# Kernel tuning notes

Measured on AMD Instinct MI355X. Metric: run time of the kernel, lower is better.

## Reference

```python
import jax, jax.numpy as jnp
import numpy as np

EPS = 1e-9
LDIM = 4  # dim_g + dim_t + dim_b + dim_w


def _mvn_logpdf(v, F):
    # batched zero-mean multivariate normal log-density, v: (N,O), F: (N,O,O)
    chol = jnp.linalg.cholesky(F)
    z = jax.scipy.linalg.solve_triangular(chol, v[..., None], lower=True)[..., 0]
    quad = jnp.sum(z * z, axis=-1)
    logdet = 2.0 * jnp.sum(jnp.log(jnp.diagonal(chol, axis1=-2, axis2=-1)), axis=-1)
    k = v.shape[-1]
    return -0.5 * (quad + logdet + k * jnp.log(2.0 * jnp.pi))


def _forward(y, B_G, B_T, B_B, B_W, lambda_r1_free, lambda_r2_free,
             q_diag, r_diag, gamma1, gamma2_learnable):
    N, Nt, O = y.shape
    L = LDIM
    # ----- _build_matrices -----
    B11 = jnp.zeros((L, L)).at[0, 0].set(B_G[0, 0]).at[1, 1].set(B_T[0, 0]).at[2, 2].set(B_B[0, 0])
    B22 = jnp.zeros((L, L)).at[3, 3].set(B_W[0, 0])
    B12 = jnp.zeros((L, L)).at[3, :3].set(1.0 / 3.0)  # regime1 factors feed shared factor
    B21 = jnp.zeros((L, L))
    L1 = jnp.zeros((O, L))
    L1 = L1.at[0, 0].set(1.0).at[1, 0].set(lambda_r1_free[0]).at[2, 0].set(lambda_r1_free[1])
    L1 = L1.at[3, 1].set(1.0).at[4, 1].set(lambda_r1_free[2]).at[5, 1].set(lambda_r1_free[3])
    L1 = L1.at[6, 2].set(1.0).at[7, 2].set(lambda_r1_free[4]).at[8, 2].set(lambda_r1_free[5])
    L2 = jnp.zeros((O, L)).at[0, 3].set(1.0).at[1:, 3].set(lambda_r2_free)
    Q = jnp.diag(jnp.abs(q_diag) + 1e-4)
    R = jnp.diag(jnp.abs(r_diag) + 1e-4)
    F_JIT = 1e-5 * jnp.eye(O)
    I_L = jnp.eye(L)
    P22_CONST = 0.9999

    # ----- initial beliefs ('informative') -----
    prob0 = jnp.tile(jnp.array([0.99, 0.01], jnp.float32), (N, 1))
    eta0 = jnp.zeros((N, L), y.dtype)
    P0 = jnp.tile(jnp.diag(jnp.array([1000.0, 1000.0, 1000.0, 1e-9], y.dtype))[None], (N, 1, 1))

    def predict(B, eta, P):
        # eta: (N,L), P: (N,L,L)
        return eta @ B.T, jnp.einsum('ij,njk,lk->nil', B, P, B) + Q

    def innov(Lm, e, Pp, y_t):
        v = y_t - e @ Lm.T
        F = jnp.einsum('oi,nij,pj->nop', Lm, Pp, Lm) + R + F_JIT
        return v, F

    def kupdate(e, Pp, Lm, v, F):
        LP = jnp.einsum('oi,nij->noj', Lm, Pp)          # (N,O,L)
        K = jnp.swapaxes(jnp.linalg.solve(F, LP), -1, -2)  # P Lm^T F^{-1}, (N,L,O)
        e_u = e + jnp.einsum('nlo,no->nl', K, v)
        IKL = I_L - K @ Lm                                # (N,L,L)
        P_u = IKL @ Pp @ jnp.swapaxes(IKL, -1, -2) + jnp.einsum('nlo,op,nmp->nlm', K, R, K)
        return e_u, P_u

    def collapse(w_a, w_b, e_a, e_b, P_a, P_b):
        e = w_a[:, None] * e_a + w_b[:, None] * e_b
        da, db = e_a - e, e_b - e
        P = (w_a[:, None, None] * (P_a + da[:, :, None] * da[:, None, :])
             + w_b[:, None, None] * (P_b + db[:, :, None] * db[:, None, :]))
        return e, P

    def step(carry, y_t):
        prob, eta1, eta2, P1, P2, ll = carry
        # HMM transition: p11 depends on regime-1 state (first L-1 components)
        logit_p11 = gamma1 + eta1[:, :3] @ gamma2_learnable
        p11 = jax.nn.sigmoid(logit_p11)
        # predictions for the 4 regime transitions (origin -> destination)
        e11, Pp11 = predict(B11, eta1, P1)
        e12, Pp12 = predict(B21, eta2, P2)
        e21, Pp21 = predict(B12, eta1, P1)
        e22, Pp22 = predict(B22, eta2, P2)
        v11, F11 = innov(L1, e11, Pp11, y_t)
        v12, F12 = innov(L1, e12, Pp12, y_t)
        v21, F21 = innov(L2, e21, Pp21, y_t)
        v22, F22 = innov(L2, e22, Pp22, y_t)
        ll11 = _mvn_logpdf(v11, F11)
        ll12 = _mvn_logpdf(v12, F12)
        ll21 = _mvn_logpdf(v21, F21)
        ll22 = _mvn_logpdf(v22, F22)
        lp = jnp.log(prob + EPS)
        c11 = lp[:, 0] + jnp.log(p11 + EPS) + ll11
        c12 = lp[:, 1] + np.log(1.0 - P22_CONST + EPS) + ll12
        c21 = lp[:, 0] + jnp.log(1.0 - p11 + EPS) + ll21
        c22 = lp[:, 1] + np.log(P22_CONST + EPS) + ll22
        logp = jnp.stack([c11, c12, c21, c22], axis=1)
        ll_t = jax.scipy.special.logsumexp(logp, axis=1)
        pt = jnp.exp(logp - ll_t[:, None])
        pr1 = pt[:, 0] + pt[:, 1]
        pr2 = pt[:, 2] + pt[:, 3]
        W11 = pt[:, 0] / (pr1 + EPS)
        W12 = pt[:, 1] / (pr1 + EPS)
        W21 = pt[:, 2] / (pr2 + EPS)
        W22 = pt[:, 3] / (pr2 + EPS)
        eu11, Pu11 = kupdate(e11, Pp11, L1, v11, F11)
        eu12, Pu12 = kupdate(e12, Pp12, L1, v12, F12)
        eu21, Pu21 = kupdate(e21, Pp21, L2, v21, F21)
        eu22, Pu22 = kupdate(e22, Pp22, L2, v22, F22)
        eta1n, P1n = collapse(W11, W12, eu11, eu12, Pu11, Pu12)
        eta2n, P2n = collapse(W21, W22, eu21, eu22, Pu21, Pu22)
        probn = jnp.stack([pr1, pr2], axis=1)
        return (probn, eta1n, eta2n, P1n, P2n, ll + ll_t.sum()), None

    carry0 = (prob0, eta0, eta0, P0, P0, jnp.zeros((), y.dtype))
    (_, _, _, _, _, total_ll), _ = jax.lax.scan(step, carry0, jnp.swapaxes(y, 0, 1))
    return total_ll


def setup_inputs() -> dict:
    key = jax.random.key(0)
    ks = jax.random.split(key, 12)
    N, Nt, O = 16384, 64, 9
    f32 = jnp.float32
    return {
        'y': jax.random.normal(ks[0], (N, Nt, O), f32),
        'B_G': jax.random.uniform(ks[1], (1, 1), f32, 0.6, 0.95),  # Beta(5,1.5)-like AR coeffs
        'B_T': jax.random.uniform(ks[2], (1, 1), f32, 0.6, 0.95),
        'B_B': jax.random.uniform(ks[3], (1, 1), f32, 0.6, 0.95),
        'B_W': jax.random.uniform(ks[4], (1, 1), f32, 0.6, 0.95),
        'lambda_r1_free': jax.random.normal(ks[5], (6,), f32),
        'lambda_r2_free': jax.random.normal(ks[6], (O - 1,), f32),
        'q_diag': jax.random.uniform(ks[7], (LDIM,), f32),
        'r_diag': jax.random.uniform(ks[8], (O,), f32),
        'gamma1': jnp.abs(jax.random.normal(ks[9], (), f32)),
        'gamma2_learnable': jax.random.normal(ks[10], (LDIM - 1,), f32),
    }


def reference(y, B_G, B_T, B_B, B_W, lambda_r1_free, lambda_r2_free,
              q_diag, r_diag, gamma1, gamma2_learnable):
    return _forward(y, B_G, B_T, B_B, B_W, lambda_r1_free, lambda_r2_free,
                    q_diag, r_diag, gamma1, gamma2_learnable)
```

## Files before the change

### kernel.cpp

```cpp
#include <hip/hip_runtime.h>


static __device__ __forceinline__ float frcp(float x)  { return __builtin_amdgcn_rcpf(x); }
static __device__ __forceinline__ float frsq(float x)  { return __builtin_amdgcn_rsqf(x); }
static __device__ __forceinline__ float fexp2(float x) { return __builtin_amdgcn_exp2f(x); }
static __device__ __forceinline__ float flog2(float x) { return __builtin_amdgcn_logf(x); }

#define EPSF   1e-9f
#define L2E    1.4426950408889634f
#define LN2    0.6931471805599453f
#define L2_2PI_9 23.86346461225016f
#define C12F   1.00001e-4f
#define P22F   0.99990001f
#define QK     (-0.5f * L2E)

__global__ __launch_bounds__(64, 1)
void kf_kernel(const float* __restrict__ y,
               const float* __restrict__ pBG, const float* __restrict__ pBT,
               const float* __restrict__ pBB, const float* __restrict__ pBW,
               const float* __restrict__ lam1, const float* __restrict__ lam2,
               const float* __restrict__ qd,  const float* __restrict__ rd,
               const float* __restrict__ pG1, const float* __restrict__ pG2,
               float* __restrict__ partial, int N, int Nt)
{
    const int lane = threadIdx.x;
    const int sid  = blockIdx.x * 64 + lane;
    const bool valid = (sid < N);
    const int rowlen = Nt * 9;

    const float bg = pBG[0], bt = pBT[0], bb = pBB[0], bw = pBW[0];
    const float a1 = lam1[0], a2 = lam1[1];
    const float a4 = lam1[2], a5 = lam1[3];
    const float a7 = lam1[4], a8 = lam1[5];
    float l2v[9], id[9], ld[9];
    l2v[0] = 1.f;
    #pragma unroll
    for (int i = 0; i < 8; ++i) l2v[i + 1] = lam2[i];
    float l2detD = 0.f;
    #pragma unroll
    for (int o = 0; o < 9; ++o) {
        float dv = fabsf(rd[o]) + 1.0e-4f + 1.0e-5f;
        id[o] = 1.0f / dv;
        ld[o] = l2v[o] * id[o];
        l2detD += flog2(dv);
    }
    const float id0 = id[0], id1 = id[1], id2 = id[2],
                id3 = id[3], id4 = id[4], id5 = id[5],
                id6 = id[6], id7 = id[7], id8 = id[8];
    const float ld0 = ld[0], ld1 = ld[1], ld2 = ld[2],
                ld3 = ld[3], ld4 = ld[4], ld5 = ld[5],
                ld6 = ld[6], ld7 = ld[7], ld8 = ld[8];
    const float aid0 = id0,      aid1 = a1 * id1, aid2 = a2 * id2;
    const float aid3 = id3,      aid4 = a4 * id4, aid5 = a5 * id5;
    const float aid6 = id6,      aid7 = a7 * id7, aid8 = a8 * id8;
    const float q0 = fabsf(qd[0]) + 1e-4f, q1 = fabsf(qd[1]) + 1e-4f;
    const float q2 = fabsf(qd[2]) + 1e-4f, q3 = fabsf(qd[3]) + 1e-4f;
    const float g0 = id0 + a1*a1*id1 + a2*a2*id2;
    const float g1 = id3 + a4*a4*id4 + a5*a5*id5;
    const float g2 = id6 + a7*a7*id7 + a8*a8*id8;
    float h = 0.f;
    #pragma unroll
    for (int o = 0; o < 9; ++o) h += l2v[o] * ld[o];
    const float pk0 = q0 / (1.f + q0 * g0);
    const float pk1 = q1 / (1.f + q1 * g1);
    const float pk2 = q2 / (1.f + q2 * g2);
    const float C12D = C12F * frsq((1.f + q0*g0) * (1.f + q1*g1) * (1.f + q2*g2));
    const float gam1 = pG1[0], w0c = pG2[0], w1c = pG2[1], w2c = pG2[2];
    const float CC = -0.5f * (l2detD + L2_2PI_9);
    const float bg2 = bg*bg, bt2 = bt*bt, bb2 = bb*bb, bw2 = bw*bw;
    const float bgbt = bg*bt, bgbb = bg*bb, btbb = bt*bb;

    float pf1 = 0.99f + EPSF, pf2 = 0.01f + EPSF;
    float se0 = 0.f, se1 = 0.f, se2 = 0.f;
    float p00 = 1000.f, p01 = 0.f, p02 = 0.f, p11 = 1000.f, p12 = 0.f, p22 = 1000.f;
    float sm2 = 0.f, sp2 = 1e-9f;
    float acc2 = 0.f;

    const float* row = y + (size_t)(valid ? sid : 0) * rowlen;
    float A[9], B[9];
    #pragma unroll
    for (int k = 0; k < 9; ++k) A[k] = row[k];

    auto step = [&](const float (&Y)[9]) {
        float logit = gam1 + w0c*se0 + w1c*se1 + w2c*se2;
        float p11s = frcp(1.f + fexp2(-logit * L2E));
        float pf11 = p11s + EPSF, pf21 = 1.f - p11s + EPSF;

        float e0 = bg*se0, e1 = bt*se1, e2 = bb*se2;
        float s00 = bg2*p00 + q0, s11 = bt2*p11 + q1, s22 = bb2*p22 + q2;
        float s01 = bgbt*p01, s02 = bgbb*p02, s12 = btbb*p12;

        float v0 = Y[0] - e0,    v1 = Y[1] - a1*e0, v2 = Y[2] - a2*e0;
        float v3 = Y[3] - e1,    v4 = Y[4] - a4*e1, v5 = Y[5] - a5*e1;
        float v6 = Y[6] - e2,    v7 = Y[7] - a7*e2, v8 = Y[8] - a8*e2;
        float u0 = aid0*v0 + aid1*v1 + aid2*v2;
        float u1 = aid3*v3 + aid4*v4 + aid5*v5;
        float u2 = aid6*v6 + aid7*v7 + aid8*v8;
        float vdv = (id0*v0)*v0 + (id1*v1)*v1 + (id2*v2)*v2
                  + (id3*v3)*v3 + (id4*v4)*v4 + (id5*v5)*v5
                  + (id6*v6)*v6 + (id7*v7)*v7 + (id8*v8)*v8;
        float yl  = ld0*Y[0] + ld1*Y[1] + ld2*Y[2]
                  + ld3*Y[3] + ld4*Y[4] + ld5*Y[5]
                  + ld6*Y[6] + ld7*Y[7] + ld8*Y[8];
        float k0 = 2.f*u0 + g0*e0, k1 = 2.f*u1 + g1*e1, k2 = 2.f*u2 + g2*e2;
        float ydy = vdv + e0*k0 + e1*k1 + e2*k2;

        float m00 = s00*g0 + 1.f, m01 = s01*g1,       m02 = s02*g2;
        float m10 = s01*g0,       m11 = s11*g1 + 1.f, m12 = s12*g2;
        float m20 = s02*g0,       m21 = s12*g1,       m22 = s22*g2 + 1.f;
        float c00 = m11*m22 - m12*m21;
        float c01 = m12*m20 - m10*m22;
        float c02 = m10*m21 - m11*m20;
        float c10 = m02*m21 - m01*m22;
        float c11 = m00*m22 - m02*m20;
        float c12 = m01*m20 - m00*m21;
        float c20 = m01*m12 - m02*m11;
        float c21 = m02*m10 - m00*m12;
        float c22 = m00*m11 - m01*m10;
        float det = m00*c00 + m01*c01 + m02*c02;
        float rs  = frsq(det);
        float iM  = rs * rs;
        float Ci00 = (s00*c00 + s01*c10 + s02*c20) * iM;
        float Ci01 = (s00*c01 + s01*c11 + s02*c21) * iM;
        float Ci02 = (s00*c02 + s01*c12 + s02*c22) * iM;
        float Ci11 = (s01*c01 + s11*c11 + s12*c21) * iM;
        float Ci12 = (s01*c02 + s11*c12 + s12*c22) * iM;
        float Ci22 = (s02*c02 + s12*c12 + s22*c22) * iM;

        float t0 = Ci00*u0 + Ci01*u1 + Ci02*u2;
        float t1 = Ci01*u0 + Ci11*u1 + Ci12*u2;
        float t2 = Ci02*u0 + Ci12*u1 + Ci22*u2;
        float quad11 = vdv - (u0*t0 + u1*t1 + u2*t2);
        float eu0 = e0 + t0, eu1 = e1 + t1, eu2 = e2 + t2;

        float u120 = u0 + g0*e0, u121 = u1 + g1*e1, u122 = u2 + g2*e2;
        float f0 = pk0*u120, f1 = pk1*u121, f2 = pk2*u122;
        float quad12 = ydy - (f0*u120 + f1*u121 + f2*u122);

        float seS = se0 + se1 + se2;
        float sPs = p00 + p11 + p22 + 2.f*(p01 + p02 + p12);
        float m2a = seS * (1.f/3.f);
        float m2b = bw * sm2;
        float pva = q3 + sPs * (1.f/9.f);
        float pvb = bw2*sp2 + q3;
        float u1a = yl - m2a*h;
        float u1b = yl - m2b*h;
        float vdaa = ydy - m2a*(2.f*yl - m2a*h);
        float vdab = ydy - m2b*(2.f*yl - m2b*h);
        float rva = frsq(1.f + pva*h);
        float rvb = frsq(1.f + pvb*h);
        float pua = pva*(rva*rva);
        float pub = pvb*(rvb*rvb);
        float quad21 = vdaa - pua*u1a*u1a;
        float quad22 = vdab - pub*u1b*u1b;
        float eua = m2a + pua*u1a;
        float eub = m2b + pub*u1b;

        float q11e = QK*quad11, q12e = QK*quad12;
        float q21e = QK*quad21, q22e = QK*quad22;
        float Mq = fmaxf(fmaxf(q11e, q12e), fmaxf(q21e, q22e));
        float w11 = pf1*pf11*rs   * fexp2(q11e - Mq);
        float w12 = pf2*C12D      * fexp2(q12e - Mq);
        float w21 = pf1*pf21*rva  * fexp2(q21e - Mq);
        float w22 = pf2*P22F*rvb  * fexp2(q22e - Mq);
        float ssum = (w11 + w12) + (w21 + w22);
        acc2 += Mq + flog2(ssum);
        float pr1n = w11 + w12, pr2n = w21 + w22;
        float inv1 = frcp(pr1n + EPSF*ssum);
        float inv2 = frcp(pr2n + EPSF*ssum);
        float issum = frcp(ssum);
        float W11 = w11*inv1, W12 = w12*inv1;
        float W21 = w21*inv2, W22 = w22*inv2;
        pf1 = pr1n*issum + EPSF;
        pf2 = pr2n*issum + EPSF;

        float ne0 = W11*eu0 + W12*f0;
        float ne1 = W11*eu1 + W12*f1;
        float ne2 = W11*eu2 + W12*f2;
        float da0 = eu0-ne0, da1 = eu1-ne1, da2 = eu2-ne2;
        float db0 = f0-ne0,  db1 = f1-ne1,  db2 = f2-ne2;
        p00 = W11*(Ci00 + da0*da0) + W12*(pk0 + db0*db0);
        p01 = W11*(Ci01 + da0*da1) + W12*(db0*db1);
        p02 = W11*(Ci02 + da0*da2) + W12*(db0*db2);
        p11 = W11*(Ci11 + da1*da1) + W12*(pk1 + db1*db1);
        p12 = W11*(Ci12 + da1*da2) + W12*(db1*db2);
        p22 = W11*(Ci22 + da2*da2) + W12*(pk2 + db2*db2);
        se0 = ne0; se1 = ne1; se2 = ne2;

        float nm2 = W21*eua + W22*eub;
        float dc = eua-nm2, dd = eub-nm2;
        sp2 = W21*(pua + dc*dc) + W22*(pub + dd*dd);
        sm2 = nm2;
    };

    for (int t = 0; t < Nt; t += 2) {
        #pragma unroll
        for (int k = 0; k < 9; ++k) B[k] = row[(t+1)*9 + k];
        step(A);
        if (t + 2 < Nt) {
            #pragma unroll
            for (int k = 0; k < 9; ++k) A[k] = row[(t+2)*9 + k];
        }
        step(B);
    }

    float acc = valid ? (acc2 + (float)Nt * CC) * LN2 : 0.f;
    #pragma unroll
    for (int off = 32; off; off >>= 1) acc += __shfl_down(acc, off, 64);
    if (lane == 0) partial[blockIdx.x] = acc;
}

__global__ __launch_bounds__(64)
void reduce_k(const float* __restrict__ part, float* __restrict__ out, int nb)
{
    float s = 0.f;
    for (int i = threadIdx.x; i < nb; i += 64) s += part[i];
    #pragma unroll
    for (int off = 32; off; off >>= 1) s += __shfl_down(s, off, 64);
    if (threadIdx.x == 0) out[0] = s;
}

extern "C" void kernel_launch(void* const* d_in, const int* in_sizes, int n_in,
                              void* d_out, int out_size, void* d_ws, size_t ws_size,
                              hipStream_t stream)
{
    const float* y    = (const float*)d_in[0];
    const float* pBG  = (const float*)d_in[1];
    const float* pBT  = (const float*)d_in[2];
    const float* pBB  = (const float*)d_in[3];
    const float* pBW  = (const float*)d_in[4];
    const float* lam1 = (const float*)d_in[5];
    const float* lam2 = (const float*)d_in[6];
    const float* qd   = (const float*)d_in[7];
    const float* rd   = (const float*)d_in[8];
    const float* pG1  = (const float*)d_in[9];
    const float* pG2  = (const float*)d_in[10];

    const int total = in_sizes[0];
    const int Nt = 64, O = 9;
    const int N = total / (Nt * O);
    const int blocks = (N + 63) / 64;

    float* partial = (float*)d_ws;
    kf_kernel<<<blocks, 64, 0, stream>>>(y, pBG, pBT, pBB, pBW, lam1, lam2,
                                         qd, rd, pG1, pG2, partial, N, Nt);
    reduce_k<<<1, 64, 0, stream>>>(partial, (float*)d_out, blocks);
}
```

Before: 130.4 us.

## Precompute state-independent observation terms off the recurrence and use packed float2 math

```diff
diff --git a/kernel.cpp b/kernel.cpp
--- a/kernel.cpp
+++ b/kernel.cpp
@@ -1,10 +1,15 @@
 #include <hip/hip_runtime.h>
 
+
+typedef float v2f __attribute__((ext_vector_type(2)));
+typedef v2f v2fu __attribute__((aligned(4)));
 
 static __device__ __forceinline__ float frcp(float x)  { return __builtin_amdgcn_rcpf(x); }
 static __device__ __forceinline__ float frsq(float x)  { return __builtin_amdgcn_rsqf(x); }
 static __device__ __forceinline__ float fexp2(float x) { return __builtin_amdgcn_exp2f(x); }
 static __device__ __forceinline__ float flog2(float x) { return __builtin_amdgcn_logf(x); }
+static __device__ __forceinline__ v2f sp(float x) { return (v2f){x, x}; }
+static __device__ __forceinline__ v2f rsq2(v2f a) { return (v2f){frsq(a.x), frsq(a.y)}; }
 
 #define EPSF   1e-9f
 #define L2E    1.4426950408889634f
@@ -44,20 +49,19 @@
         ld[o] = l2v[o] * id[o];
         l2detD += flog2(dv);
     }
-    const float id0 = id[0], id1 = id[1], id2 = id[2],
-                id3 = id[3], id4 = id[4], id5 = id[5],
-                id6 = id[6], id7 = id[7], id8 = id[8];
-    const float ld0 = ld[0], ld1 = ld[1], ld2 = ld[2],
-                ld3 = ld[3], ld4 = ld[4], ld5 = ld[5],
-                ld6 = ld[6], ld7 = ld[7], ld8 = ld[8];
-    const float aid0 = id0,      aid1 = a1 * id1, aid2 = a2 * id2;
-    const float aid3 = id3,      aid4 = a4 * id4, aid5 = a5 * id5;
-    const float aid6 = id6,      aid7 = a7 * id7, aid8 = a8 * id8;
+    const float id8 = id[8], ld8 = ld[8];
+    const v2f idv01 = {id[0], id[1]}, idv23 = {id[2], id[3]},
+              idv45 = {id[4], id[5]}, idv67 = {id[6], id[7]};
+    const v2f ldv01 = {ld[0], ld[1]}, ldv23 = {ld[2], ld[3]},
+              ldv45 = {ld[4], ld[5]}, ldv67 = {ld[6], ld[7]};
+    const float aid0 = id[0],    aid1 = a1*id[1], aid2 = a2*id[2];
+    const float aid3 = id[3],    aid4 = a4*id[4], aid5 = a5*id[5];
+    const float aid6 = id[6],    aid7 = a7*id[7], aid8 = a8*id[8];
     const float q0 = fabsf(qd[0]) + 1e-4f, q1 = fabsf(qd[1]) + 1e-4f;
     const float q2 = fabsf(qd[2]) + 1e-4f, q3 = fabsf(qd[3]) + 1e-4f;
-    const float g0 = id0 + a1*a1*id1 + a2*a2*id2;
-    const float g1 = id3 + a4*a4*id4 + a5*a5*id5;
-    const float g2 = id6 + a7*a7*id7 + a8*a8*id8;
+    const float g0 = id[0] + a1*a1*id[1] + a2*a2*id[2];
+    const float g1 = id[3] + a4*a4*id[4] + a5*a5*id[5];
+    const float g2 = id[6] + a7*a7*id[7] + a8*a8*id[8];
     float h = 0.f;
     #pragma unroll
     for (int o = 0; o < 9; ++o) h += l2v[o] * ld[o];
@@ -69,6 +73,7 @@
     const float CC = -0.5f * (l2detD + L2_2PI_9);
     const float bg2 = bg*bg, bt2 = bt*bt, bb2 = bb*bb, bw2 = bw*bw;
     const float bgbt = bg*bt, bgbb = bg*bb, btbb = bt*bb;
+    const v2f hv = {h, h};
 
     float pf1 = 0.99f + EPSF, pf2 = 0.01f + EPSF;
     float se0 = 0.f, se1 = 0.f, se2 = 0.f;
@@ -76,132 +81,142 @@
     float sm2 = 0.f, sp2 = 1e-9f;
     float acc2 = 0.f;
 
-    const float* row = y + (size_t)(valid ? sid : 0) * rowlen;
-    float A[9], B[9];
-    #pragma unroll
-    for (int k = 0; k < 9; ++k) A[k] = row[k];
-
-    auto step = [&](const float (&Y)[9]) {
-        float logit = gam1 + w0c*se0 + w1c*se1 + w2c*se2;
-        float p11s = frcp(1.f + fexp2(-logit * L2E));
-        float pf11 = p11s + EPSF, pf21 = 1.f - p11s + EPSF;
+    struct Yr { v2f ab, cd, ef, gh; float i8; };
+    struct YB { float uy0, uy1, uy2, yl, ydy, f0, f1, f2, q12e; };
+
+    const char* rowb = (const char*)(y + (size_t)(valid ? sid : 0) * rowlen);
+    auto loadY = [&](Yr& r, int t) {
+        const char* p = rowb + t * 36;
+        r.ab = *(const v2fu*)(p);
+        r.cd = *(const v2fu*)(p + 8);
+        r.ef = *(const v2fu*)(p + 16);
+        r.gh = *(const v2fu*)(p + 24);
+        r.i8 = *(const float*)(p + 32);
+    };
+    auto computeYB = [&](const Yr& r) {
+        YB o;
+        v2f m0 = idv01*r.ab, m1 = idv23*r.cd, m2 = idv45*r.ef, m3 = idv67*r.gh;
+        v2f yq = m0*r.ab + m1*r.cd + m2*r.ef + m3*r.gh;
+        o.ydy = fmaf(id8*r.i8, r.i8, yq.x + yq.y);
+        v2f la = ldv01*r.ab + ldv23*r.cd + ldv45*r.ef + ldv67*r.gh;
+        o.yl = fmaf(ld8, r.i8, la.x + la.y);
+        o.uy0 = fmaf(aid2, r.cd.x, fmaf(aid1, r.ab.y, aid0*r.ab.x));
+        o.uy1 = fmaf(aid5, r.ef.y, fmaf(aid4, r.ef.x, aid3*r.cd.y));
+        o.uy2 = fmaf(aid8, r.i8,   fmaf(aid7, r.gh.y, aid6*r.gh.x));
+        o.f0 = pk0*o.uy0; o.f1 = pk1*o.uy1; o.f2 = pk2*o.uy2;
+        o.q12e = QK * (o.ydy - (o.f0*o.uy0 + o.f1*o.uy1 + o.f2*o.uy2));
+        return o;
+    };
+
+    auto step = [&](const YB& yb) {
+        float logit = fmaf(w2c, se2, fmaf(w1c, se1, fmaf(w0c, se0, gam1)));
+        float p11s = frcp(1.f + fexp2(-L2E * logit));
+        float pp1 = pf1 * (p11s + EPSF);
+        float pp2 = pf1 * (1.f - p11s + EPSF);
 
         float e0 = bg*se0, e1 = bt*se1, e2 = bb*se2;
-        float s00 = bg2*p00 + q0, s11 = bt2*p11 + q1, s22 = bb2*p22 + q2;
+        float s00 = fmaf(bg2, p00, q0), s11 = fmaf(bt2, p11, q1), s22 = fmaf(bb2, p22, q2);
         float s01 = bgbt*p01, s02 = bgbb*p02, s12 = btbb*p12;
 
-        float v0 = Y[0] - e0,    v1 = Y[1] - a1*e0, v2 = Y[2] - a2*e0;
-        float v3 = Y[3] - e1,    v4 = Y[4] - a4*e1, v5 = Y[5] - a5*e1;
-        float v6 = Y[6] - e2,    v7 = Y[7] - a7*e2, v8 = Y[8] - a8*e2;
-        float u0 = aid0*v0 + aid1*v1 + aid2*v2;
-        float u1 = aid3*v3 + aid4*v4 + aid5*v5;
-        float u2 = aid6*v6 + aid7*v7 + aid8*v8;
-        float vdv = (id0*v0)*v0 + (id1*v1)*v1 + (id2*v2)*v2
-                  + (id3*v3)*v3 + (id4*v4)*v4 + (id5*v5)*v5
-                  + (id6*v6)*v6 + (id7*v7)*v7 + (id8*v8)*v8;
-        float yl  = ld0*Y[0] + ld1*Y[1] + ld2*Y[2]
-                  + ld3*Y[3] + ld4*Y[4] + ld5*Y[5]
-                  + ld6*Y[6] + ld7*Y[7] + ld8*Y[8];
-        float k0 = 2.f*u0 + g0*e0, k1 = 2.f*u1 + g1*e1, k2 = 2.f*u2 + g2*e2;
-        float ydy = vdv + e0*k0 + e1*k1 + e2*k2;
-
-        float m00 = s00*g0 + 1.f, m01 = s01*g1,       m02 = s02*g2;
-        float m10 = s01*g0,       m11 = s11*g1 + 1.f, m12 = s12*g2;
-        float m20 = s02*g0,       m21 = s12*g1,       m22 = s22*g2 + 1.f;
-        float c00 = m11*m22 - m12*m21;
-        float c01 = m12*m20 - m10*m22;
-        float c02 = m10*m21 - m11*m20;
-        float c10 = m02*m21 - m01*m22;
-        float c11 = m00*m22 - m02*m20;
-        float c12 = m01*m20 - m00*m21;
-        float c20 = m01*m12 - m02*m11;
-        float c21 = m02*m10 - m00*m12;
-        float c22 = m00*m11 - m01*m10;
-        float det = m00*c00 + m01*c01 + m02*c02;
+        float u0 = fmaf(-g0, e0, yb.uy0);
+        float u1 = fmaf(-g1, e1, yb.uy1);
+        float u2 = fmaf(-g2, e2, yb.uy2);
+        float vdv = yb.ydy - (e0*(yb.uy0+u0) + e1*(yb.uy1+u1) + e2*(yb.uy2+u2));
+
+        float m00 = fmaf(s00, g0, 1.f), m11 = fmaf(s11, g1, 1.f), m22 = fmaf(s22, g2, 1.f);
+        float m01 = s01*g1, m02 = s02*g2;
+        float m10 = s01*g0, m20 = s02*g0;
+        float m12 = s12*g2, m21 = s12*g1;
+        float c00 = fmaf(m11, m22, -m12*m21);
+        float c01 = fmaf(m12, m20, -m10*m22);
+        float c02 = fmaf(m10, m21, -m11*m20);
+        float c10 = fmaf(m02, m21, -m01*m22);
+        float c11 = fmaf(m00, m22, -m02*m20);
+        float c12 = fmaf(m01, m20, -m00*m21);
+        float c20 = fmaf(m01, m12, -m02*m11);
+        float c21 = fmaf(m02, m10, -m00*m12);
+        float c22 = fmaf(m00, m11, -m01*m10);
+        float det = fmaf(m02, c02, fmaf(m01, c01, m00*c00));
         float rs  = frsq(det);
         float iM  = rs * rs;
-        float Ci00 = (s00*c00 + s01*c10 + s02*c20) * iM;
-        float Ci01 = (s00*c01 + s01*c11 + s02*c21) * iM;
-        float Ci02 = (s00*c02 + s01*c12 + s02*c22) * iM;
-        float Ci11 = (s01*c01 + s11*c11 + s12*c21) * iM;
-        float Ci12 = (s01*c02 + s11*c12 + s12*c22) * iM;
-        float Ci22 = (s02*c02 + s12*c12 + s22*c22) * iM;
-
-        float t0 = Ci00*u0 + Ci01*u1 + Ci02*u2;
-        float t1 = Ci01*u0 + Ci11*u1 + Ci12*u2;
-        float t2 = Ci02*u0 + Ci12*u1 + Ci22*u2;
-        float quad11 = vdv - (u0*t0 + u1*t1 + u2*t2);
-        float eu0 = e0 + t0, eu1 = e1 + t1, eu2 = e2 + t2;
-
-        float u120 = u0 + g0*e0, u121 = u1 + g1*e1, u122 = u2 + g2*e2;
-        float f0 = pk0*u120, f1 = pk1*u121, f2 = pk2*u122;
-        float quad12 = ydy - (f0*u120 + f1*u121 + f2*u122);
+        float SC00 = fmaf(s02, c20, fmaf(s01, c10, s00*c00));
+        float SC01 = fmaf(s02, c21, fmaf(s01, c11, s00*c01));
+        float SC02 = fmaf(s02, c22, fmaf(s01, c12, s00*c02));
+        float SC11 = fmaf(s12, c21, fmaf(s11, c11, s01*c01));
+        float SC12 = fmaf(s12, c22, fmaf(s11, c12, s01*c02));
+        float SC22 = fmaf(s22, c22, fmaf(s12, c12, s02*c02));
+
+        float n0 = fmaf(SC02, u2, fmaf(SC01, u1, SC00*u0));
+        float n1 = fmaf(SC12, u2, fmaf(SC11, u1, SC01*u0));
+        float n2 = fmaf(SC22, u2, fmaf(SC12, u1, SC02*u0));
+        float un = fmaf(u2, n2, fmaf(u1, n1, u0*n0));
+        float quad11 = fmaf(-iM, un, vdv);
+        float eu0 = fmaf(iM, n0, e0), eu1 = fmaf(iM, n1, e1), eu2 = fmaf(iM, n2, e2);
 
         float seS = se0 + se1 + se2;
-        float sPs = p00 + p11 + p22 + 2.f*(p01 + p02 + p12);
-        float m2a = seS * (1.f/3.f);
-        float m2b = bw * sm2;
-        float pva = q3 + sPs * (1.f/9.f);
-        float pvb = bw2*sp2 + q3;
-        float u1a = yl - m2a*h;
-        float u1b = yl - m2b*h;
-        float vdaa = ydy - m2a*(2.f*yl - m2a*h);
-        float vdab = ydy - m2b*(2.f*yl - m2b*h);
-        float rva = frsq(1.f + pva*h);
-        float rvb = frsq(1.f + pvb*h);
-        float pua = pva*(rva*rva);
-        float pub = pvb*(rvb*rvb);
-        float quad21 = vdaa - pua*u1a*u1a;
-        float quad22 = vdab - pub*u1b*u1b;
-        float eua = m2a + pua*u1a;
-        float eub = m2b + pub*u1b;
-
-        float q11e = QK*quad11, q12e = QK*quad12;
-        float q21e = QK*quad21, q22e = QK*quad22;
-        float Mq = fmaxf(fmaxf(q11e, q12e), fmaxf(q21e, q22e));
-        float w11 = pf1*pf11*rs   * fexp2(q11e - Mq);
-        float w12 = pf2*C12D      * fexp2(q12e - Mq);
-        float w21 = pf1*pf21*rva  * fexp2(q21e - Mq);
-        float w22 = pf2*P22F*rvb  * fexp2(q22e - Mq);
-        float ssum = (w11 + w12) + (w21 + w22);
+        float sPs = fmaf(2.f, (p01 + p02) + p12, (p00 + p11) + p22);
+        v2f m2v; m2v.x = seS * (1.f/3.f);          m2v.y = bw * sm2;
+        v2f pvv; pvv.x = fmaf(sPs, 1.f/9.f, q3);   pvv.y = fmaf(bw2, sp2, q3);
+        v2f ylv = sp(yb.yl);
+        v2f u1v = ylv - m2v*hv;
+        v2f vdav = sp(yb.ydy) - m2v*(sp(2.f*yb.yl) - m2v*hv);
+        v2f denv = sp(1.f) + pvv*hv;
+        v2f rv  = rsq2(denv);
+        v2f puv = pvv*(rv*rv);
+        v2f pu1 = puv*u1v;
+        v2f quadv = vdav - pu1*u1v;
+        v2f euv = m2v + pu1;
+
+        float q11e = QK*quad11;
+        float q21e = QK*quadv.x, q22e = QK*quadv.y;
+        float Mq = fmaxf(fmaxf(q11e, yb.q12e), fmaxf(q21e, q22e));
+        float w11 = pp1*rs        * fexp2(q11e - Mq);
+        float w12 = pf2*C12D      * fexp2(yb.q12e - Mq);
+        float w21 = pp2*rv.x      * fexp2(q21e - Mq);
+        float w22 = pf2*P22F*rv.y * fexp2(q22e - Mq);
+        float pr1n = w11 + w12, pr2n = w21 + w22;
+        float ssum = pr1n + pr2n;
         acc2 += Mq + flog2(ssum);
-        float pr1n = w11 + w12, pr2n = w21 + w22;
-        float inv1 = frcp(pr1n + EPSF*ssum);
-        float inv2 = frcp(pr2n + EPSF*ssum);
+        float inv1 = frcp(fmaf(EPSF, ssum, pr1n));
+        float inv2 = frcp(fmaf(EPSF, ssum, pr2n));
         float issum = frcp(ssum);
         float W11 = w11*inv1, W12 = w12*inv1;
         float W21 = w21*inv2, W22 = w22*inv2;
-        pf1 = pr1n*issum + EPSF;
-        pf2 = pr2n*issum + EPSF;
-
-        float ne0 = W11*eu0 + W12*f0;
-        float ne1 = W11*eu1 + W12*f1;
-        float ne2 = W11*eu2 + W12*f2;
+        pf1 = fmaf(pr1n, issum, EPSF);
+        pf2 = fmaf(pr2n, issum, EPSF);
+        float W11i = W11 * iM;
+
+        float ne0 = fmaf(W12, yb.f0, W11*eu0);
+        float ne1 = fmaf(W12, yb.f1, W11*eu1);
+        float ne2 = fmaf(W12, yb.f2, W11*eu2);
         float da0 = eu0-ne0, da1 = eu1-ne1, da2 = eu2-ne2;
-        float db0 = f0-ne0,  db1 = f1-ne1,  db2 = f2-ne2;
-        p00 = W11*(Ci00 + da0*da0) + W12*(pk0 + db0*db0);
-        p01 = W11*(Ci01 + da0*da1) + W12*(db0*db1);
-        p02 = W11*(Ci02 + da0*da2) + W12*(db0*db2);
-        p11 = W11*(Ci11 + da1*da1) + W12*(pk1 + db1*db1);
-        p12 = W11*(Ci12 + da1*da2) + W12*(db1*db2);
-        p22 = W11*(Ci22 + da2*da2) + W12*(pk2 + db2*db2);
+        float db0 = yb.f0-ne0, db1 = yb.f1-ne1, db2 = yb.f2-ne2;
+        p00 = fmaf(W12, fmaf(db0, db0, pk0), fmaf(W11, da0*da0, W11i*SC00));
+        p01 = fmaf(W12, db0*db1,             fmaf(W11, da0*da1, W11i*SC01));
+        p02 = fmaf(W12, db0*db2,             fmaf(W11, da0*da2, W11i*SC02));
+        p11 = fmaf(W12, fmaf(db1, db1, pk1), fmaf(W11, da1*da1, W11i*SC11));
+        p12 = fmaf(W12, db1*db2,             fmaf(W11, da1*da2, W11i*SC12));
+        p22 = fmaf(W12, fmaf(db2, db2, pk2), fmaf(W11, da2*da2, W11i*SC22));
         se0 = ne0; se1 = ne1; se2 = ne2;
 
-        float nm2 = W21*eua + W22*eub;
-        float dc = eua-nm2, dd = eub-nm2;
-        sp2 = W21*(pua + dc*dc) + W22*(pub + dd*dd);
+        float nm2 = fmaf(W22, euv.y, W21*euv.x);
+        v2f dcv = euv - sp(nm2);
+        v2f tv = puv + dcv*dcv;
+        sp2 = fmaf(W22, tv.y, W21*tv.x);
         sm2 = nm2;
     };
 
+    Yr A, B; YB ya, yb;
+    loadY(A, 0);
+    loadY(B, 1);
+    ya = computeYB(A);
     for (int t = 0; t < Nt; t += 2) {
-        #pragma unroll
-        for (int k = 0; k < 9; ++k) B[k] = row[(t+1)*9 + k];
-        step(A);
-        if (t + 2 < Nt) {
-            #pragma unroll
-            for (int k = 0; k < 9; ++k) A[k] = row[(t+2)*9 + k];
-        }
-        step(B);
+        step(ya);
+        yb = computeYB(B);
+        if (t + 2 < Nt) loadY(A, t + 2);
+        step(yb);
+        if (t + 2 < Nt) ya = computeYB(A);
+        if (t + 3 < Nt) loadY(B, t + 3);
     }
 
     float acc = valid ? (acc2 + (float)Nt * CC) * LN2 : 0.f;
```

Result: faster. 127.6 us (-2.2%).
